# Optimization experiments

Hardware: AMD Instinct MI355X
Metric: run time of the kernel (lower is better)

The kernel has to match this reference:

```python
import jax, jax.numpy as jnp
import numpy as np
from jax import lax

B, H, W = 64, 64, 64
N_CHANNELS = 16
N_FILTERS = 128
N_DENSE = 256
T_STEPS = 60  # update_time() with Tmin=60, Tmax=61


def setup_inputs() -> dict:
    key = jax.random.key(0)
    ks = jax.random.split(key, 7)
    s_conv = 1.0 / np.sqrt(3 * 3 * N_CHANNELS)
    s_d1 = 1.0 / np.sqrt(N_FILTERS)
    s_d2 = 1.0 / np.sqrt(N_DENSE)
    return {
        "input": jax.random.uniform(ks[0], (B, H, W), dtype=jnp.float32),
        # conv kernel in HWIO layout for lax.conv_general_dilated
        "conv_w": jax.random.uniform(ks[1], (3, 3, N_CHANNELS, N_FILTERS), jnp.float32, -s_conv, s_conv),
        "conv_b": jax.random.uniform(ks[2], (N_FILTERS,), jnp.float32, -s_conv, s_conv),
        "w1": jax.random.uniform(ks[3], (N_FILTERS, N_DENSE), jnp.float32, -s_d1, s_d1),
        "b1": jax.random.uniform(ks[4], (N_DENSE,), jnp.float32, -s_d1, s_d1),
        "w2": jax.random.uniform(ks[5], (N_DENSE, N_CHANNELS), jnp.float32, -s_d2, s_d2),
        "b2": jax.random.uniform(ks[6], (N_CHANNELS,), jnp.float32, -s_d2, s_d2),
    }


def reference(input, conv_w, conv_b, w1, b1, w2, b2):
    # grid: (B,H,W,C), channel 0 seeded with the input image
    grid = jnp.zeros((B, H, W, N_CHANNELS), dtype=input.dtype)
    grid = grid.at[..., 0].set(input)
    # zero channel 0 of the delta (channel 0 is frozen)
    ch_mask = (jnp.arange(N_CHANNELS) != 0).astype(input.dtype)  # (C,)

    def step(g, _):
        conv = lax.conv_general_dilated(
            g, conv_w, window_strides=(1, 1), padding="SAME",
            dimension_numbers=("NHWC", "HWIO", "NHWC")) + conv_b
        h = jax.nn.relu(conv)                       # (B,H,W,F)
        d = jax.nn.relu(h @ w1 + b1) @ w2 + b2      # (B,H,W,C)
        alive = (g[..., 0:1] > 0.1).astype(g.dtype)  # (B,H,W,1)
        g = g + d * ch_mask * alive
        return g, None

    grid, _ = lax.scan(step, grid, None, length=T_STEPS)
    return jax.nn.softmax(grid[..., 1:11], axis=-1)  # (B,H,W,10)
```

## Files before the change

### kernel.cpp

```cpp
#include <hip/hip_runtime.h>
#include <math.h>

typedef _Float16 f16;
typedef f16  f16x8 __attribute__((ext_vector_type(8)));
typedef f16  f16x4 __attribute__((ext_vector_type(4)));
typedef float f32x4 __attribute__((ext_vector_type(4)));

#define NB 64
#define NC 16
#define NF 128
#define ND 256
#define NSTEP 60
#define GRID_ELEMS (NB*64*64*NC)
#define NPIX (NB*64*64)

#define KCONV 160
#define HSS   136
#define RPS   20

#define OFF_CW 0
#define OFF_W1 20480
#define OFF_W2 53248

__global__ void init_grid(const float* __restrict__ inp, float* __restrict__ g) {
    int i = blockIdx.x * 256 + threadIdx.x;
    if (i >= GRID_ELEMS) return;
    int c = i & 15;
    g[i] = (c == 0) ? inp[i >> 4] : 0.0f;
}

__global__ void prep_weights(const float* __restrict__ cw, const float* __restrict__ w1,
                             const float* __restrict__ w2, f16* __restrict__ wb) {
    int i = blockIdx.x * 256 + threadIdx.x;
    float v; int off, idx;
    if (i < 20480) {
        int f = i / 160, k = i - f * 160;
        v = (k < 144) ? cw[k * 128 + f] : 0.0f;
        off = OFF_CW; idx = i;
    } else if (i < 20480 + 32768) {
        int r = i - 20480;
        int j = r >> 7, f = r & 127;
        v = w1[f * 256 + j];
        off = OFF_W1; idx = r;
    } else {
        int r = i - 20480 - 32768;
        int c = r >> 8, j = r & 255;
        v = w2[j * 16 + c];
        off = OFF_W2; idx = r;
    }
    wb[off + idx] = (f16)v;
}

__global__ __launch_bounds__(256, 3) void nca_step(
    const float* __restrict__ gin, float* __restrict__ gout,
    const f16* __restrict__ wb,
    const float* __restrict__ cb, const float* __restrict__ b1, const float* __restrict__ b2)
{
    __shared__ f16 smem[20480];
    f16* const hs   = smem;
    f16* const un   = smem + 17408;
    f16* const halo = un;
    f16* const aScr = un;
    float* const redF = (float*)smem;

    const int t    = threadIdx.x;
    const int w    = t >> 6;
    const int lane = t & 63;
    const int q    = lane >> 4;
    const int l16  = lane & 15;

    const int bi = blockIdx.x;
    const int b  = bi >> 5;
    const int tl = bi & 31;
    const int y0 = (tl >> 2) << 3;
    const int x0 = (tl & 3) << 4;

    const float* gb  = gin  + (size_t)b * 64 * 64 * 16;
    float*       gob = gout + (size_t)b * 64 * 64 * 16;

    const int fbase = w << 5;
    f16x8 cA[2][5];
    #pragma unroll
    for (int ft = 0; ft < 2; ++ft)
        #pragma unroll
        for (int kc = 0; kc < 5; ++kc)
            cA[ft][kc] = *(const f16x8*)(wb + OFF_CW +
                (size_t)(fbase + ft * 16 + l16) * KCONV + kc * 32 + q * 8);
    const int jbase = w << 6;
    f16x8 w2f[2];
    #pragma unroll
    for (int jp = 0; jp < 2; ++jp)
        w2f[jp] = *(const f16x8*)(wb + OFF_W2 + (size_t)l16 * 256 + jbase + jp * 32 + q * 8);

    for (int i = t; i < 720; i += 256) {
        int c4 = (i & 3) << 2;
        int xy = i >> 2;
        int xx = xy % 18;
        int yy = xy / 18;
        int gy = y0 + yy - 1, gx = x0 + xx - 1;
        f32x4 v = {0.f, 0.f, 0.f, 0.f};
        if ((unsigned)gy < 64u && (unsigned)gx < 64u)
            v = *(const f32x4*)(gb + (gy * 64 + gx) * 16 + c4);
        f16x4 hv;
        hv.x = (f16)v.x; hv.y = (f16)v.y; hv.z = (f16)v.z; hv.w = (f16)v.w;
        *(f16x4*)(halo + (yy * 18 + xx) * 16 + c4) = hv;
    }
    __syncthreads();

    f32x4 acc[2][8];
    #pragma unroll
    for (int ft = 0; ft < 2; ++ft) {
        f32x4 bias;
        bias.x = cb[fbase + ft * 16 + q * 4 + 0];
        bias.y = cb[fbase + ft * 16 + q * 4 + 1];
        bias.z = cb[fbase + ft * 16 + q * 4 + 2];
        bias.w = cb[fbase + ft * 16 + q * 4 + 3];
        #pragma unroll
        for (int p = 0; p < 8; ++p) acc[ft][p] = bias;
    }

    #pragma unroll
    for (int kc = 0; kc < 5; ++kc) {
        int tap = kc * 2 + (q >> 1);
        if (tap > 8) tap = 8;
        int dy = tap / 3, dx = tap - dy * 3;
        int boff = dy * 288 + (l16 + dx) * 16 + (q & 1) * 8;
        #pragma unroll
        for (int p = 0; p < 8; ++p) {
            f16x8 bf = *(const f16x8*)(halo + boff + p * 288);
            #pragma unroll
            for (int ft = 0; ft < 2; ++ft)
                acc[ft][p] = __builtin_amdgcn_mfma_f32_16x16x32_f16(cA[ft][kc], bf, acc[ft][p], 0, 0, 0);
        }
    }

    #pragma unroll
    for (int ft = 0; ft < 2; ++ft)
        #pragma unroll
        for (int p = 0; p < 8; ++p) {
            f32x4 a = acc[ft][p];
            f16x4 pk;
            pk.x = (f16)fmaxf(a.x, 0.0f);
            pk.y = (f16)fmaxf(a.y, 0.0f);
            pk.z = (f16)fmaxf(a.z, 0.0f);
            pk.w = (f16)fmaxf(a.w, 0.0f);
            *(f16x4*)(hs + (p * 16 + l16) * HSS + fbase + ft * 16 + q * 4) = pk;
        }
    __syncthreads();

    f16x8 dA[2][2][4];
    float b1v[2][2][4];
    #pragma unroll
    for (int jp = 0; jp < 2; ++jp)
        #pragma unroll
        for (int jt2 = 0; jt2 < 2; ++jt2) {
            #pragma unroll
            for (int kc = 0; kc < 4; ++kc)
                dA[jp][jt2][kc] = *(const f16x8*)(wb + OFF_W1 +
                    (size_t)(jbase + jp * 32 + jt2 * 16 + l16) * 128 + kc * 32 + q * 8);
            #pragma unroll
            for (int r = 0; r < 4; ++r)
                b1v[jp][jt2][r] = b1[jbase + jp * 32 + jt2 * 16 + q * 4 + r];
        }

    f32x4 dacc[8];
    #pragma unroll
    for (int p = 0; p < 8; ++p) { dacc[p].x = 0.f; dacc[p].y = 0.f; dacc[p].z = 0.f; dacc[p].w = 0.f; }

    f16* const myScr = aScr + (w * 16 + l16) * 40;

    for (int p = 0; p < 8; ++p) {
        f16x8 hB[4];
        #pragma unroll
        for (int kc = 0; kc < 4; ++kc)
            hB[kc] = *(const f16x8*)(hs + (p * 16 + l16) * HSS + kc * 32 + q * 8);

        #pragma unroll
        for (int jp = 0; jp < 2; ++jp) {
            #pragma unroll
            for (int jt2 = 0; jt2 < 2; ++jt2) {
                f32x4 a1;
                a1.x = b1v[jp][jt2][0]; a1.y = b1v[jp][jt2][1];
                a1.z = b1v[jp][jt2][2]; a1.w = b1v[jp][jt2][3];
                #pragma unroll
                for (int kc = 0; kc < 4; ++kc)
                    a1 = __builtin_amdgcn_mfma_f32_16x16x32_f16(dA[jp][jt2][kc], hB[kc], a1, 0, 0, 0);
                f16x4 pk;
                pk.x = (f16)fmaxf(a1.x, 0.0f);
                pk.y = (f16)fmaxf(a1.y, 0.0f);
                pk.z = (f16)fmaxf(a1.z, 0.0f);
                pk.w = (f16)fmaxf(a1.w, 0.0f);
                *(f16x4*)(myScr + jt2 * 16 + q * 4) = pk;
            }
            f16x8 af = *(const f16x8*)(myScr + q * 8);
            dacc[p] = __builtin_amdgcn_mfma_f32_16x16x32_f16(af, w2f[jp], dacc[p], 0, 0, 0);
        }
    }

    __syncthreads();
    #pragma unroll
    for (int p = 0; p < 8; ++p)
        #pragma unroll
        for (int r = 0; r < 4; ++r) {
            int px = p * 16 + q * 4 + r;
            redF[(w * 128 + px) * RPS + l16] = dacc[p][r];
        }
    __syncthreads();

    {
        const int px = t >> 1;
        const int c0 = (t & 1) * 8;
        const int yy = px >> 4, xx = px & 15;
        const size_t pixb = ((size_t)(y0 + yy) * 64 + (x0 + xx)) * 16;
        const float a0 = gb[pixb];
        const bool alive = (a0 > 0.1f);
        #pragma unroll
        for (int h = 0; h < 2; ++h) {
            const int ch = c0 + h * 4;
            f32x4 v0 = *(const f32x4*)(redF + (0 * 128 + px) * RPS + ch);
            f32x4 v1 = *(const f32x4*)(redF + (1 * 128 + px) * RPS + ch);
            f32x4 v2 = *(const f32x4*)(redF + (2 * 128 + px) * RPS + ch);
            f32x4 v3 = *(const f32x4*)(redF + (3 * 128 + px) * RPS + ch);
            f32x4 sv = v0 + v1 + v2 + v3;
            f32x4 gv = *(const f32x4*)(gb + pixb + ch);
            f32x4 ov;
            #pragma unroll
            for (int i = 0; i < 4; ++i) {
                int c = ch + i;
                float nv = gv[i];
                if (alive && c != 0) nv += sv[i] + b2[c];
                ov[i] = nv;
            }
            *(f32x4*)(gob + pixb + ch) = ov;
        }
    }
}

__global__ void softmax_out(const float* __restrict__ g, float* __restrict__ out) {
    int pix = blockIdx.x * 256 + threadIdx.x;
    if (pix >= NPIX) return;
    const float* gp = g + (size_t)pix * 16;
    float v[10];
    float m = -1e30f;
    #pragma unroll
    for (int i = 0; i < 10; ++i) { v[i] = gp[1 + i]; m = fmaxf(m, v[i]); }
    float s = 0.f;
    #pragma unroll
    for (int i = 0; i < 10; ++i) { v[i] = __expf(v[i] - m); s += v[i]; }
    float inv = 1.0f / s;
    float* op = out + (size_t)pix * 10;
    #pragma unroll
    for (int i = 0; i < 10; ++i) op[i] = v[i] * inv;
}

extern "C" void kernel_launch(void* const* d_in, const int* in_sizes, int n_in,
                              void* d_out, int out_size, void* d_ws, size_t ws_size,
                              hipStream_t stream) {
    const float* inp = (const float*)d_in[0];
    const float* cw  = (const float*)d_in[1];
    const float* cb  = (const float*)d_in[2];
    const float* w1  = (const float*)d_in[3];
    const float* b1  = (const float*)d_in[4];
    const float* w2  = (const float*)d_in[5];
    const float* b2  = (const float*)d_in[6];
    float* out = (float*)d_out;

    float* g0 = (float*)d_ws;
    float* g1 = g0 + GRID_ELEMS;
    f16* wb = (f16*)d_out;

    prep_weights<<<224, 256, 0, stream>>>(cw, w1, w2, wb);
    init_grid<<<(GRID_ELEMS + 255) / 256, 256, 0, stream>>>(inp, g0);

    float* bufs[2] = { g0, g1 };
    for (int s = 0; s < NSTEP; ++s) {
        nca_step<<<2048, 256, 0, stream>>>(bufs[s & 1], bufs[(s + 1) & 1],
                                           wb, cb, b1, b2);
    }
    softmax_out<<<(NPIX + 255) / 256, 256, 0, stream>>>(g0, out);
}
```

Measured before the change: 2.705 ms.

## Shrink per-block tile to 8x8 pixels and pad shared-memory strides

Each block now handles an 8x8 pixel tile instead of 8x16, so the launch grid doubles to 4096 blocks and shared memory per block shrinks from about 40KB to 22KB. The halo layout gets a padded per-pixel stride of 24 halves, and the reduction buffer stride changes to 17 floats, both aimed at cutting LDS bank conflicts. The smaller footprint is meant to allow more resident blocks and better load balance. In exchange, halo overhead per output pixel rises, and per-block weight loads from global memory are repeated twice as often. The stride-17 f32x4 LDS accesses are also no longer 16-byte aligned.

```diff
diff --git a/kernel.cpp b/kernel.cpp
--- a/kernel.cpp
+++ b/kernel.cpp
@@ -16,7 +16,8 @@
 
 #define KCONV 160
 #define HSS   136
-#define RPS   20
+#define HCS   24
+#define RPS   17
 
 #define OFF_CW 0
 #define OFF_W1 20480
@@ -56,9 +57,9 @@
     const f16* __restrict__ wb,
     const float* __restrict__ cb, const float* __restrict__ b1, const float* __restrict__ b2)
 {
-    __shared__ f16 smem[20480];
+    __shared__ f16 smem[11264];
     f16* const hs   = smem;
-    f16* const un   = smem + 17408;
+    f16* const un   = smem + 8704;
     f16* const halo = un;
     f16* const aScr = un;
     float* const redF = (float*)smem;
@@ -70,10 +71,9 @@
     const int l16  = lane & 15;
 
     const int bi = blockIdx.x;
-    const int b  = bi >> 5;
-    const int tl = bi & 31;
-    const int y0 = (tl >> 2) << 3;
-    const int x0 = (tl & 3) << 4;
+    const int b  = bi >> 6;
+    const int y0 = ((bi >> 3) & 7) << 3;
+    const int x0 = (bi & 7) << 3;
 
     const float* gb  = gin  + (size_t)b * 64 * 64 * 16;
     float*       gob = gout + (size_t)b * 64 * 64 * 16;
@@ -92,22 +92,22 @@
     for (int jp = 0; jp < 2; ++jp)
         w2f[jp] = *(const f16x8*)(wb + OFF_W2 + (size_t)l16 * 256 + jbase + jp * 32 + q * 8);
 
-    for (int i = t; i < 720; i += 256) {
+    for (int i = t; i < 400; i += 256) {
         int c4 = (i & 3) << 2;
         int xy = i >> 2;
-        int xx = xy % 18;
-        int yy = xy / 18;
+        int xx = xy % 10;
+        int yy = xy / 10;
         int gy = y0 + yy - 1, gx = x0 + xx - 1;
         f32x4 v = {0.f, 0.f, 0.f, 0.f};
         if ((unsigned)gy < 64u && (unsigned)gx < 64u)
             v = *(const f32x4*)(gb + (gy * 64 + gx) * 16 + c4);
         f16x4 hv;
         hv.x = (f16)v.x; hv.y = (f16)v.y; hv.z = (f16)v.z; hv.w = (f16)v.w;
-        *(f16x4*)(halo + (yy * 18 + xx) * 16 + c4) = hv;
-    }
-    __syncthreads();
-
-    f32x4 acc[2][8];
+        *(f16x4*)(halo + xy * HCS + c4) = hv;
+    }
+    __syncthreads();
+
+    f32x4 acc[2][4];
     #pragma unroll
     for (int ft = 0; ft < 2; ++ft) {
         f32x4 bias;
@@ -116,7 +116,7 @@
         bias.z = cb[fbase + ft * 16 + q * 4 + 2];
         bias.w = cb[fbase + ft * 16 + q * 4 + 3];
         #pragma unroll
-        for (int p = 0; p < 8; ++p) acc[ft][p] = bias;
+        for (int p = 0; p < 4; ++p) acc[ft][p] = bias;
     }
 
     #pragma unroll
@@ -124,10 +124,11 @@
         int tap = kc * 2 + (q >> 1);
         if (tap > 8) tap = 8;
         int dy = tap / 3, dx = tap - dy * 3;
-        int boff = dy * 288 + (l16 + dx) * 16 + (q & 1) * 8;
-        #pragma unroll
-        for (int p = 0; p < 8; ++p) {
-            f16x8 bf = *(const f16x8*)(halo + boff + p * 288);
+        #pragma unroll
+        for (int p = 0; p < 4; ++p) {
+            int yy = p * 2 + (l16 >> 3) + dy;
+            int xx = (l16 & 7) + dx;
+            f16x8 bf = *(const f16x8*)(halo + (yy * 10 + xx) * HCS + (q & 1) * 8);
             #pragma unroll
             for (int ft = 0; ft < 2; ++ft)
                 acc[ft][p] = __builtin_amdgcn_mfma_f32_16x16x32_f16(cA[ft][kc], bf, acc[ft][p], 0, 0, 0);
@@ -137,7 +138,7 @@
     #pragma unroll
     for (int ft = 0; ft < 2; ++ft)
         #pragma unroll
-        for (int p = 0; p < 8; ++p) {
+        for (int p = 0; p < 4; ++p) {
             f32x4 a = acc[ft][p];
             f16x4 pk;
             pk.x = (f16)fmaxf(a.x, 0.0f);
@@ -163,13 +164,13 @@
                 b1v[jp][jt2][r] = b1[jbase + jp * 32 + jt2 * 16 + q * 4 + r];
         }
 
-    f32x4 dacc[8];
-    #pragma unroll
-    for (int p = 0; p < 8; ++p) { dacc[p].x = 0.f; dacc[p].y = 0.f; dacc[p].z = 0.f; dacc[p].w = 0.f; }
+    f32x4 dacc[4];
+    #pragma unroll
+    for (int p = 0; p < 4; ++p) { dacc[p].x = 0.f; dacc[p].y = 0.f; dacc[p].z = 0.f; dacc[p].w = 0.f; }
 
     f16* const myScr = aScr + (w * 16 + l16) * 40;
 
-    for (int p = 0; p < 8; ++p) {
+    for (int p = 0; p < 4; ++p) {
         f16x8 hB[4];
         #pragma unroll
         for (int kc = 0; kc < 4; ++kc)
@@ -199,40 +200,36 @@
 
     __syncthreads();
     #pragma unroll
-    for (int p = 0; p < 8; ++p)
+    for (int p = 0; p < 4; ++p)
         #pragma unroll
         for (int r = 0; r < 4; ++r) {
             int px = p * 16 + q * 4 + r;
-            redF[(w * 128 + px) * RPS + l16] = dacc[p][r];
+            redF[(w * 64 + px) * RPS + l16] = dacc[p][r];
         }
     __syncthreads();
 
     {
-        const int px = t >> 1;
-        const int c0 = (t & 1) * 8;
-        const int yy = px >> 4, xx = px & 15;
+        const int px = t >> 2;
+        const int cq = (t & 3) << 2;
+        const int yy = px >> 3, xx = px & 7;
         const size_t pixb = ((size_t)(y0 + yy) * 64 + (x0 + xx)) * 16;
         const float a0 = gb[pixb];
         const bool alive = (a0 > 0.1f);
-        #pragma unroll
-        for (int h = 0; h < 2; ++h) {
-            const int ch = c0 + h * 4;
-            f32x4 v0 = *(const f32x4*)(redF + (0 * 128 + px) * RPS + ch);
-            f32x4 v1 = *(const f32x4*)(redF + (1 * 128 + px) * RPS + ch);
-            f32x4 v2 = *(const f32x4*)(redF + (2 * 128 + px) * RPS + ch);
-            f32x4 v3 = *(const f32x4*)(redF + (3 * 128 + px) * RPS + ch);
-            f32x4 sv = v0 + v1 + v2 + v3;
-            f32x4 gv = *(const f32x4*)(gb + pixb + ch);
-            f32x4 ov;
-            #pragma unroll
-            for (int i = 0; i < 4; ++i) {
-                int c = ch + i;
-                float nv = gv[i];
-                if (alive && c != 0) nv += sv[i] + b2[c];
-                ov[i] = nv;
-            }
-            *(f32x4*)(gob + pixb + ch) = ov;
-        }
+        f32x4 s0 = *(const f32x4*)(redF + (0 * 64 + px) * RPS + cq);
+        f32x4 s1 = *(const f32x4*)(redF + (1 * 64 + px) * RPS + cq);
+        f32x4 s2 = *(const f32x4*)(redF + (2 * 64 + px) * RPS + cq);
+        f32x4 s3 = *(const f32x4*)(redF + (3 * 64 + px) * RPS + cq);
+        f32x4 sv = s0 + s1 + s2 + s3;
+        f32x4 gv = *(const f32x4*)(gb + pixb + cq);
+        f32x4 ov;
+        #pragma unroll
+        for (int i = 0; i < 4; ++i) {
+            int c = cq + i;
+            float nv = gv[i];
+            if (alive && c != 0) nv += sv[i] + b2[c];
+            ov[i] = nv;
+        }
+        *(f32x4*)(gob + pixb + cq) = ov;
     }
 }
 
@@ -274,7 +271,7 @@
 
     float* bufs[2] = { g0, g1 };
     for (int s = 0; s < NSTEP; ++s) {
-        nca_step<<<2048, 256, 0, stream>>>(bufs[s & 1], bufs[(s + 1) & 1],
+        nca_step<<<4096, 256, 0, stream>>>(bufs[s & 1], bufs[(s + 1) & 1],
                                            wb, cb, b1, b2);
     }
     softmax_out<<<(NPIX + 255) / 256, 256, 0, stream>>>(g0, out);
```

Result: slower. 3.696 ms (+36.6%).
